# Performance work log

Measured on AMD Instinct MI355X. Metric: run time of the kernel, lower is better.

## Reference

```python
import jax, jax.numpy as jnp
import numpy as np


def setup_inputs() -> dict:
    key = jax.random.key(0)
    ks = jax.random.split(key, 7)
    N, E, D_IN, D_OUT = 50000, 800000, 128, 128
    features = jax.random.normal(ks[0], (N, D_IN), dtype=jnp.float32)
    src = jax.random.randint(ks[1], (E,), 0, N, dtype=jnp.int64)
    dst = jax.random.randint(ks[2], (E,), 0, N, dtype=jnp.int64)
    W1 = jax.random.normal(ks[3], (D_OUT, D_IN), dtype=jnp.float32) * (1.0 / np.sqrt(D_IN))
    b1 = jax.random.normal(ks[4], (D_OUT,), dtype=jnp.float32) * 0.01
    W2 = jax.random.normal(ks[5], (1, 2 * D_OUT), dtype=jnp.float32) * (1.0 / np.sqrt(2 * D_OUT))
    b2 = jax.random.normal(ks[6], (1,), dtype=jnp.float32) * 0.01
    return {"features": features, "src": src, "dst": dst,
            "W1": W1, "b1": b1, "W2": W2, "b2": b2}


def reference(features, src, dst, W1, b1, W2, b2):
    # Gather endpoint features per edge: [E, D_in]
    f_src = features[src]
    f_dst = features[dst]
    # Shared linear projection (torch Linear: x @ W.T + b) -> [E, D_out]
    h_src = jnp.einsum('ed,od->eo', f_src, W1) + b1
    h_dst = jnp.einsum('ed,od->eo', f_dst, W1) + b1
    # Concat [diff, sum] -> [E, 2*D_out]; dropout is identity at inference
    e_feats = jnp.concatenate([h_src - h_dst, h_src + h_dst], axis=1)
    # Final linear to scalar per edge, squeeze, tanh -> [E]
    out = jnp.tanh((jnp.einsum('ef,of->eo', e_feats, W2) + b2).squeeze(-1))
    return out
```

## Files before the change

### kernel.cpp

```cpp
#include <hip/hip_runtime.h>
#include <math.h>

#define D 128

__global__ void prep_kernel(const float* __restrict__ W1, const float* __restrict__ b1,
                            const float* __restrict__ W2, const float* __restrict__ b2,
                            float* __restrict__ uvc) {
    int d = threadIdx.x;
    float u = 0.f, v = 0.f;
    for (int o = 0; o < D; ++o) {
        float wa = W2[o];
        float wb = W2[D + o];
        float w1 = W1[o * D + d];
        u += (wa + wb) * w1;
        v += (wb - wa) * w1;
    }
    uvc[d] = u;
    uvc[D + d] = v;
    if (d == 0) {
        float c = b2[0];
        for (int o = 0; o < D; ++o) c += 2.f * W2[D + o] * b1[o];
        uvc[2 * D] = c;
    }
}

__global__ void node_kernel(const float* __restrict__ feat, const float* __restrict__ uvc,
                            float* __restrict__ s, float* __restrict__ t, int N) {
    int wave = (int)((blockIdx.x * blockDim.x + threadIdx.x) >> 6);
    int lane = threadIdx.x & 63;
    if (wave >= N) return;
    float2 fv = ((const float2*)(feat + (size_t)wave * D))[lane];
    float2 uu = ((const float2*)uvc)[lane];
    float2 vv = ((const float2*)(uvc + D))[lane];
    float su = fv.x * uu.x + fv.y * uu.y;
    float sv = fv.x * vv.x + fv.y * vv.y;
    #pragma unroll
    for (int off = 32; off; off >>= 1) {
        su += __shfl_xor(su, off, 64);
        sv += __shfl_xor(sv, off, 64);
    }
    if (lane == 0) { s[wave] = su; t[wave] = sv; }
}

__global__ void edge_kernel(const int* __restrict__ src, const int* __restrict__ dst,
                            const float* __restrict__ s, const float* __restrict__ t,
                            const float* __restrict__ uvc, float* __restrict__ out, int E) {
    int i = blockIdx.x * blockDim.x + threadIdx.x;
    int e0 = i * 4;
    if (e0 >= E) return;
    float c = uvc[2 * D];
    if (e0 + 3 < E) {
        int4 si = ((const int4*)src)[i];
        int4 di = ((const int4*)dst)[i];
        float4 r;
        r.x = tanhf(s[si.x] + t[di.x] + c);
        r.y = tanhf(s[si.y] + t[di.y] + c);
        r.z = tanhf(s[si.z] + t[di.z] + c);
        r.w = tanhf(s[si.w] + t[di.w] + c);
        ((float4*)out)[i] = r;
    } else {
        for (int e = e0; e < E; ++e)
            out[e] = tanhf(s[src[e]] + t[dst[e]] + c);
    }
}

__global__ void fused_edge_kernel(const float* __restrict__ feat,
                                  const int* __restrict__ src, const int* __restrict__ dst,
                                  const float* __restrict__ uvc, float* __restrict__ out, int E) {
    int wave = (int)((blockIdx.x * blockDim.x + threadIdx.x) >> 6);
    int lane = threadIdx.x & 63;
    if (wave >= E) return;
    int sn = src[wave], dn = dst[wave];
    float2 fs = ((const float2*)(feat + (size_t)sn * D))[lane];
    float2 fd = ((const float2*)(feat + (size_t)dn * D))[lane];
    float2 uu = ((const float2*)uvc)[lane];
    float2 vv = ((const float2*)(uvc + D))[lane];
    float acc = fs.x * uu.x + fs.y * uu.y + fd.x * vv.x + fd.y * vv.y;
    #pragma unroll
    for (int off = 32; off; off >>= 1) acc += __shfl_xor(acc, off, 64);
    if (lane == 0) out[wave] = tanhf(acc + uvc[2 * D]);
}

extern "C" void kernel_launch(void* const* d_in, const int* in_sizes, int n_in,
                              void* d_out, int out_size, void* d_ws, size_t ws_size,
                              hipStream_t stream) {
    const float* feat = (const float*)d_in[0];
    const int*   src  = (const int*)d_in[1];
    const int*   dst  = (const int*)d_in[2];
    const float* W1   = (const float*)d_in[3];
    const float* b1   = (const float*)d_in[4];
    const float* W2   = (const float*)d_in[5];
    const float* b2   = (const float*)d_in[6];
    float* out = (float*)d_out;

    int N = in_sizes[0] / D;
    int E = in_sizes[1];

    float* uvc = (float*)d_ws;
    float* s   = uvc + 512;
    float* t   = s + N;
    size_t needed = (512 + 2 * (size_t)N) * sizeof(float);

    prep_kernel<<<1, D, 0, stream>>>(W1, b1, W2, b2, uvc);

    if (ws_size >= needed) {
        int nblocks = (N + 3) / 4;
        node_kernel<<<nblocks, 256, 0, stream>>>(feat, uvc, s, t, N);
        int nthreads = (E + 3) / 4;
        edge_kernel<<<(nthreads + 255) / 256, 256, 0, stream>>>(src, dst, s, t, uvc, out, E);
    } else {
        int nblocks = (E + 3) / 4;
        fused_edge_kernel<<<nblocks, 256, 0, stream>>>(feat, src, dst, uvc, out, E);
    }
}
```

Before: 104.5 us.

## Interleave node scalars, parallelize prep over 512 threads, two nodes per wave

The prep kernel now splits the 128-output reduction across four thread groups and combines the partial sums in shared memory. The u and v vectors are stored interleaved. Node scalars s and t are packed into one float2 array, so the edge gathers read 8-byte entries from a single array instead of 4-byte entries from two arrays. The node kernel handles two nodes per wave with float4 loads and a shorter shuffle reduction. The edge kernel now gathers 8 bytes per endpoint where it needs only 4, which may add memory traffic on random accesses.

Result: faster. 95.13 us (-9.0%).

```diff
diff --git a/kernel.cpp b/kernel.cpp
--- a/kernel.cpp
+++ b/kernel.cpp
@@ -3,48 +3,67 @@
 
 #define D 128
 
+
 __global__ void prep_kernel(const float* __restrict__ W1, const float* __restrict__ b1,
                             const float* __restrict__ W2, const float* __restrict__ b2,
                             float* __restrict__ uvc) {
-    int d = threadIdx.x;
+    __shared__ float su[4 * D];
+    __shared__ float sv[4 * D];
+    __shared__ float sc[D];
+    int tid = threadIdx.x;
+    int d = tid & (D - 1);
+    int ch = tid >> 7;
     float u = 0.f, v = 0.f;
-    for (int o = 0; o < D; ++o) {
+    int o0 = ch * 32;
+    #pragma unroll 8
+    for (int k = 0; k < 32; ++k) {
+        int o = o0 + k;
         float wa = W2[o];
         float wb = W2[D + o];
         float w1 = W1[o * D + d];
         u += (wa + wb) * w1;
         v += (wb - wa) * w1;
     }
-    uvc[d] = u;
-    uvc[D + d] = v;
-    if (d == 0) {
-        float c = b2[0];
-        for (int o = 0; o < D; ++o) c += 2.f * W2[D + o] * b1[o];
-        uvc[2 * D] = c;
+    su[ch * D + d] = u;
+    sv[ch * D + d] = v;
+    if (ch == 0) sc[d] = 2.f * W2[D + d] * b1[d];
+    __syncthreads();
+    if (tid < D) {
+        float uu = su[d] + su[D + d] + su[2 * D + d] + su[3 * D + d];
+        float vv = sv[d] + sv[D + d] + sv[2 * D + d] + sv[3 * D + d];
+        uvc[2 * d]     = uu;
+        uvc[2 * d + 1] = vv;
+    } else if (tid == D) {
+        float cc = b2[0];
+        for (int o = 0; o < D; ++o) cc += sc[o];
+        uvc[2 * D] = cc;
     }
 }
 
 __global__ void node_kernel(const float* __restrict__ feat, const float* __restrict__ uvc,
-                            float* __restrict__ s, float* __restrict__ t, int N) {
+                            float2* __restrict__ st, int N) {
     int wave = (int)((blockIdx.x * blockDim.x + threadIdx.x) >> 6);
     int lane = threadIdx.x & 63;
-    if (wave >= N) return;
-    float2 fv = ((const float2*)(feat + (size_t)wave * D))[lane];
-    float2 uu = ((const float2*)uvc)[lane];
-    float2 vv = ((const float2*)(uvc + D))[lane];
-    float su = fv.x * uu.x + fv.y * uu.y;
-    float sv = fv.x * vv.x + fv.y * vv.y;
+    int half = lane >> 5;
+    int l = lane & 31;
+    int node = wave * 2 + half;
+    if (node >= N) return;
+    float4 f = ((const float4*)(feat + (size_t)node * D))[l];
+    float4 a = ((const float4*)uvc)[2 * l];
+    float4 b = ((const float4*)uvc)[2 * l + 1];
+    float s = f.x * a.x + f.y * a.z + f.z * b.x + f.w * b.z;
+    float t = f.x * a.y + f.y * a.w + f.z * b.y + f.w * b.w;
     #pragma unroll
-    for (int off = 32; off; off >>= 1) {
-        su += __shfl_xor(su, off, 64);
-        sv += __shfl_xor(sv, off, 64);
+    for (int off = 16; off; off >>= 1) {
+        s += __shfl_xor(s, off, 64);
+        t += __shfl_xor(t, off, 64);
     }
-    if (lane == 0) { s[wave] = su; t[wave] = sv; }
+    if (l == 0) st[node] = make_float2(s, t);
 }
 
 __global__ void edge_kernel(const int* __restrict__ src, const int* __restrict__ dst,
-                            const float* __restrict__ s, const float* __restrict__ t,
-                            const float* __restrict__ uvc, float* __restrict__ out, int E) {
+                            const float2* __restrict__ st, const float* __restrict__ uvc,
+                            float* __restrict__ out, int E) {
     int i = blockIdx.x * blockDim.x + threadIdx.x;
     int e0 = i * 4;
     if (e0 >= E) return;
@@ -52,15 +71,17 @@
     if (e0 + 3 < E) {
         int4 si = ((const int4*)src)[i];
         int4 di = ((const int4*)dst)[i];
+        float2 a0 = st[si.x], a1 = st[si.y], a2 = st[si.z], a3 = st[si.w];
+        float2 b0 = st[di.x], b1v = st[di.y], b2v = st[di.z], b3 = st[di.w];
         float4 r;
-        r.x = tanhf(s[si.x] + t[di.x] + c);
-        r.y = tanhf(s[si.y] + t[di.y] + c);
-        r.z = tanhf(s[si.z] + t[di.z] + c);
-        r.w = tanhf(s[si.w] + t[di.w] + c);
+        r.x = tanhf(a0.x + b0.y + c);
+        r.y = tanhf(a1.x + b1v.y + c);
+        r.z = tanhf(a2.x + b2v.y + c);
+        r.w = tanhf(a3.x + b3.y + c);
         ((float4*)out)[i] = r;
     } else {
         for (int e = e0; e < E; ++e)
-            out[e] = tanhf(s[src[e]] + t[dst[e]] + c);
+            out[e] = tanhf(st[src[e]].x + st[dst[e]].y + c);
     }
 }
 
@@ -73,9 +94,9 @@
     int sn = src[wave], dn = dst[wave];
     float2 fs = ((const float2*)(feat + (size_t)sn * D))[lane];
     float2 fd = ((const float2*)(feat + (size_t)dn * D))[lane];
-    float2 uu = ((const float2*)uvc)[lane];
-    float2 vv = ((const float2*)(uvc + D))[lane];
-    float acc = fs.x * uu.x + fs.y * uu.y + fd.x * vv.x + fd.y * vv.y;
+    float2 p = ((const float2*)uvc)[2 * lane];
+    float2 q = ((const float2*)uvc)[2 * lane + 1];
+    float acc = fs.x * p.x + fs.y * q.x + fd.x * p.y + fd.y * q.y;
     #pragma unroll
     for (int off = 32; off; off >>= 1) acc += __shfl_xor(acc, off, 64);
     if (lane == 0) out[wave] = tanhf(acc + uvc[2 * D]);
@@ -97,17 +118,16 @@
     int E = in_sizes[1];
 
     float* uvc = (float*)d_ws;
-    float* s   = uvc + 512;
-    float* t   = s + N;
+    float2* st = (float2*)((float*)d_ws + 512);
     size_t needed = (512 + 2 * (size_t)N) * sizeof(float);
 
-    prep_kernel<<<1, D, 0, stream>>>(W1, b1, W2, b2, uvc);
+    prep_kernel<<<1, 512, 0, stream>>>(W1, b1, W2, b2, uvc);
 
     if (ws_size >= needed) {
-        int nblocks = (N + 3) / 4;
-        node_kernel<<<nblocks, 256, 0, stream>>>(feat, uvc, s, t, N);
+        int nblocks = (N + 7) / 8;
+        node_kernel<<<nblocks, 256, 0, stream>>>(feat, uvc, st, N);
         int nthreads = (E + 3) / 4;
-        edge_kernel<<<(nthreads + 255) / 256, 256, 0, stream>>>(src, dst, s, t, uvc, out, E);
+        edge_kernel<<<(nthreads + 255) / 256, 256, 0, stream>>>(src, dst, st, uvc, out, E);
     } else {
         int nblocks = (E + 3) / 4;
         fused_edge_kernel<<<nblocks, 256, 0, stream>>>(feat, src, dst, uvc, out, E);
```
